# Kernel tuning notes

Measured on AMD Instinct MI355X. Metric: run time of the kernel, lower is better.

## Reference

```python
import jax, jax.numpy as jnp
import numpy as np

B, S, H = 2, 1024, 1024
NH, HD = 8, 128
E, TOPK, MI = 8, 2, 1024
SI = 2 * MI  # shared experts intermediate (n_shared_experts=2)
EPS = 1e-6
THETA = 10000.0


def setup_inputs() -> dict:
    key = jax.random.key(0)
    ks = jax.random.split(key, 16)
    w = lambda k, shp: (0.02 * jax.random.normal(k, shp, dtype=jnp.float32))
    # RoPE tables [S, HD]
    inv_freq = 1.0 / (THETA ** (np.arange(0, HD, 2, dtype=np.float32) / HD))
    t = np.arange(S, dtype=np.float32)
    freqs = np.outer(t, inv_freq)
    emb = np.concatenate([freqs, freqs], axis=-1)
    return {
        "hidden_states": jax.random.normal(ks[0], (B, S, H), dtype=jnp.float32),
        "ln1_w": jnp.ones((H,), jnp.float32),
        "ln2_w": jnp.ones((H,), jnp.float32),
        "q_w": w(ks[1], (H, H)),
        "k_w": w(ks[2], (H, H)),
        "v_w": w(ks[3], (H, H)),
        "o_w": w(ks[4], (H, H)),
        "cos": jnp.asarray(np.cos(emb), jnp.float32),
        "sin": jnp.asarray(np.sin(emb), jnp.float32),
        "gate_w": w(ks[5], (E, H)),
        "eg_w": w(ks[6], (E, MI, H)),
        "eu_w": w(ks[7], (E, MI, H)),
        "ed_w": w(ks[8], (E, H, MI)),
        "sg_w": w(ks[9], (SI, H)),
        "su_w": w(ks[10], (SI, H)),
        "sd_w": w(ks[11], (H, SI)),
    }


def _rmsnorm(x, w):
    return x * jax.lax.rsqrt(jnp.mean(x * x, axis=-1, keepdims=True) + EPS) * w


def _rotate_half(x):
    x1, x2 = jnp.split(x, 2, axis=-1)
    return jnp.concatenate([-x2, x1], axis=-1)


def _attention(x, q_w, k_w, v_w, o_w, cos, sin):
    b, s, h = x.shape
    q = (x @ q_w.T).reshape(b, s, NH, HD)
    k = (x @ k_w.T).reshape(b, s, NH, HD)
    v = (x @ v_w.T).reshape(b, s, NH, HD)
    c = cos[None, :s, None, :]
    sn = sin[None, :s, None, :]
    q = q * c + _rotate_half(q) * sn
    k = k * c + _rotate_half(k) * sn
    scores = jnp.einsum("bqhd,bkhd->bhqk", q, k) / jnp.sqrt(jnp.float32(HD))
    causal = jnp.tril(jnp.ones((s, s), dtype=bool))
    scores = jnp.where(causal[None, None], scores, -jnp.inf)
    p = jax.nn.softmax(scores, axis=-1)
    out = jnp.einsum("bhqk,bkhd->bqhd", p, v).reshape(b, s, h)
    return out @ o_w.T


def _mlp(x, gw, uw, dw):
    return (jax.nn.silu(x @ gw.T) * (x @ uw.T)) @ dw.T


def _moe(x, gate_w, eg_w, eu_w, ed_w, sg_w, su_w, sd_w):
    b, s, h = x.shape
    xt = x.reshape(-1, h)                              # [T, H]
    T = xt.shape[0]
    probs = jax.nn.softmax(xt @ gate_w.T, axis=-1)     # [T, E]
    rw, idx = jax.lax.top_k(probs, TOPK)               # [T, K]
    rw = rw / (jnp.sum(rw, axis=-1, keepdims=True) + 1e-20)  # norm_topk_prob
    # dense combine weights [T, E] (zero for unselected experts)
    w_full = jnp.zeros((T, E), xt.dtype).at[jnp.arange(T)[:, None], idx].add(rw)
    # dense all-expert compute, masked-combined (faithful to per-token loop math)
    g = jax.nn.silu(jnp.einsum("th,eih->tei", xt, eg_w))
    u = jnp.einsum("th,eih->tei", xt, eu_w)
    y = jnp.einsum("tei,ehi->teh", g * u, ed_w)        # [T, E, H]
    routed = jnp.einsum("teh,te->th", y, w_full)
    shared = _mlp(xt, sg_w, su_w, sd_w)
    return (routed + shared).reshape(b, s, h)


def reference(hidden_states, ln1_w, ln2_w, q_w, k_w, v_w, o_w, cos, sin,
              gate_w, eg_w, eu_w, ed_w, sg_w, su_w, sd_w):
    x = hidden_states
    x = x + _attention(_rmsnorm(x, ln1_w), q_w, k_w, v_w, o_w, cos, sin)
    x = x + _moe(_rmsnorm(x, ln2_w), gate_w, eg_w, eu_w, ed_w, sg_w, su_w, sd_w)
    return x
```

## Files before the change

### kernel.cpp

```cpp
#include <hip/hip_runtime.h>

#define B_   2
#define S_   1024
#define H_   1024
#define NH_  8
#define HD_  128
#define E_   8
#define MI_  1024
#define SI_  2048
#define T_   2048
#define CAP_ 2048

typedef unsigned short u16;
typedef __attribute__((ext_vector_type(4))) float f32x4;
typedef __attribute__((ext_vector_type(4))) unsigned short u16x4;
typedef __attribute__((ext_vector_type(8))) unsigned short u16x8;
typedef __attribute__((ext_vector_type(8))) __bf16 bf16x8;

__device__ __forceinline__ u16 f2bf(float f) {
  unsigned int u = __builtin_bit_cast(unsigned int, f);
  u = (u + 0x7fffu + ((u >> 16) & 1u)) >> 16;
  return (u16)u;
}
__device__ __forceinline__ float bf2f(u16 u) {
  return __builtin_bit_cast(float, (unsigned int)u << 16);
}
__device__ __forceinline__ float wave_sum(float v) {
#pragma unroll
  for (int o = 32; o; o >>= 1) v += __shfl_down(v, o, 64);
  return v;
}
__device__ __forceinline__ void gll16(const u16* g, u16* l) {
  __builtin_amdgcn_global_load_lds((const __attribute__((address_space(1))) void*)g,
                                   (__attribute__((address_space(3))) void*)l, 16, 0, 0);
}

__device__ __forceinline__ void cvt_moe_rows(
    int row0, int tid,
    const float* __restrict__ eg_w, const float* __restrict__ eu_w,
    const float* __restrict__ ed_w, const float* __restrict__ sg_w,
    const float* __restrict__ su_w, const float* __restrict__ sd_w,
    u16* __restrict__ egu, u16* __restrict__ edb,
    u16* __restrict__ sgu, u16* __restrict__ sdb) {
  const float* src[8];
  u16* dst[8];
#pragma unroll
  for (int g = 0; g < 8; g++) {
    int row = row0 + g;
    if (row < 20480) {
      int rel = row - 4096;
      int zu = rel >= 8192;
      int r = rel & 8191;
      int e = r >> 10, i = r & 1023;
      int orow = (i >> 4) * 32 + (i & 15) + (zu ? 16 : 0);
      src[g] = (zu ? eu_w : eg_w) + (long)r * 1024;
      dst[g] = egu + ((long)e * 2048 + orow) * 1024;
    } else if (row < 28672) {
      long f = (long)(row - 20480) * 1024;
      src[g] = ed_w + f;
      dst[g] = edb + f;
    } else if (row < 32768) {
      int rel = row - 28672;
      int zu = rel >= 2048;
      int i = rel & 2047;
      int orow = (i >> 4) * 32 + (i & 15) + (zu ? 16 : 0);
      src[g] = (zu ? su_w : sg_w) + (long)i * 1024;
      dst[g] = sgu + (long)orow * 1024;
    } else {
      long f = (long)(row - 32768) * 1024;
      src[g] = sd_w + f;
      dst[g] = sdb + f;
    }
  }
  f32x4 v[8];
#pragma unroll
  for (int g = 0; g < 8; g++)
    v[g] = __builtin_nontemporal_load((const f32x4*)src[g] + tid);
#pragma unroll
  for (int g = 0; g < 8; g++) {
    u16x4 o;
#pragma unroll
    for (int c = 0; c < 4; c++) o[c] = f2bf(v[g][c]);
    ((u16x4*)dst[g])[tid] = o;
  }
}

__global__ void cvt_all(const float* __restrict__ q_w, const float* __restrict__ k_w,
                        const float* __restrict__ v_w, const float* __restrict__ o_w,
                        u16* __restrict__ qwb,
                        const float* __restrict__ hidden, const float* __restrict__ ln1w,
                        u16* __restrict__ xn) {
  int bid = blockIdx.x, tid = threadIdx.x;
  if (bid >= 512) {
    int t = bid - 512;
    f32x4 v = ((const f32x4*)(hidden + (long)t * H_))[tid];
    float ss = v[0]*v[0] + v[1]*v[1] + v[2]*v[2] + v[3]*v[3];
    __shared__ float red[4];
    float s = wave_sum(ss);
    if ((tid & 63) == 0) red[tid >> 6] = s;
    __syncthreads();
    float r = rsqrtf((red[0] + red[1] + red[2] + red[3]) * (1.0f / H_) + 1e-6f);
    f32x4 wv = ((const f32x4*)ln1w)[tid];
    u16x4 o;
#pragma unroll
    for (int c = 0; c < 4; c++) o[c] = f2bf(v[c] * r * wv[c]);
    ((u16x4*)(xn + (long)t * H_))[tid] = o;
    return;
  }
  const float* src[8];
  u16* dst[8];
#pragma unroll
  for (int g = 0; g < 8; g++) {
    int row = bid * 8 + g;
    int seg = row >> 10;
    const float* in = (seg == 0) ? q_w : (seg == 1) ? k_w : (seg == 2) ? v_w : o_w;
    src[g] = in + (long)(row & 1023) * 1024;
    dst[g] = qwb + (long)row * 1024;
  }
  f32x4 v[8];
#pragma unroll
  for (int g = 0; g < 8; g++)
    v[g] = __builtin_nontemporal_load((const f32x4*)src[g] + tid);
#pragma unroll
  for (int g = 0; g < 8; g++) {
    u16x4 o;
#pragma unroll
    for (int c = 0; c < 4; c++) o[c] = f2bf(v[g][c]);
    ((u16x4*)dst[g])[tid] = o;
  }
}

__global__ void rmsnorm2_gate(const float* __restrict__ x1, const float* __restrict__ ln2w,
                              const float* __restrict__ gw, u16* __restrict__ xn,
                              int* __restrict__ eidx, float* __restrict__ aw) {
  int t = blockIdx.x, tid = threadIdx.x;
  int lane = tid & 63, wave = tid >> 6;
  f32x4 v = ((const f32x4*)(x1 + (long)t * H_))[tid];
  float ss = v[0]*v[0] + v[1]*v[1] + v[2]*v[2] + v[3]*v[3];
  __shared__ float redS[4];
  __shared__ float redE[4][E_];
  float s = wave_sum(ss);
  if (lane == 0) redS[wave] = s;
  __syncthreads();
  float r = rsqrtf((redS[0] + redS[1] + redS[2] + redS[3]) * (1.0f / H_) + 1e-6f);
  f32x4 wv = ((const f32x4*)ln2w)[tid];
  float xv[4];
  u16x4 o;
#pragma unroll
  for (int c = 0; c < 4; c++) { xv[c] = v[c] * r * wv[c]; o[c] = f2bf(xv[c]); }
  ((u16x4*)(xn + (long)t * H_))[tid] = o;
  float acc[E_];
#pragma unroll
  for (int e = 0; e < E_; e++) {
    f32x4 g = ((const f32x4*)(gw + (long)e * H_))[tid];
    acc[e] = xv[0]*g[0] + xv[1]*g[1] + xv[2]*g[2] + xv[3]*g[3];
  }
#pragma unroll
  for (int e = 0; e < E_; e++) acc[e] = wave_sum(acc[e]);
  if (lane == 0)
#pragma unroll
    for (int e = 0; e < E_; e++) redE[wave][e] = acc[e];
  __syncthreads();
  if (tid == 0) {
    float l[E_];
#pragma unroll
    for (int e = 0; e < E_; e++) l[e] = redE[0][e] + redE[1][e] + redE[2][e] + redE[3][e];
    float mx = l[0];
#pragma unroll
    for (int e = 1; e < E_; e++) mx = fmaxf(mx, l[e]);
    float p[E_], z = 0.f;
#pragma unroll
    for (int e = 0; e < E_; e++) { p[e] = __expf(l[e] - mx); z += p[e]; }
    int e0 = 0;
#pragma unroll
    for (int e = 1; e < E_; e++) if (p[e] > p[e0]) e0 = e;
    int e1 = (e0 == 0) ? 1 : 0;
#pragma unroll
    for (int e = 0; e < E_; e++) if (e != e0 && p[e] > p[e1]) e1 = e;
    float q0 = p[e0] / z, q1 = p[e1] / z;
    float invs = 1.0f / (q0 + q1 + 1e-20f);
    eidx[t * 2] = e0;
    eidx[t * 2 + 1] = e1;
    aw[t * 2] = q0 * invs;
    aw[t * 2 + 1] = q1 * invs;
  }
}

__global__ __launch_bounds__(256) void route_scan(const int* __restrict__ eidx,
                                                  int* __restrict__ arow,
                                                  int* __restrict__ cursor,
                                                  int* __restrict__ itok,
                                                  int* __restrict__ wgu,
                                                  int* __restrict__ wdn) {
  __shared__ int sc[E_][256];
  int tid = threadIdx.x;
  for (int i = tid; i < E_ * CAP_; i += 256) itok[i] = 0;
  unsigned c0 = 0, c1 = 0;
  int ebuf[16];
#pragma unroll
  for (int i = 0; i < 16; i++) {
    int e = eidx[tid * 16 + i];
    ebuf[i] = e;
    if (e < 4) c0 += 1u << (8 * e); else c1 += 1u << (8 * (e - 4));
  }
#pragma unroll
  for (int e = 0; e < E_; e++)
    sc[e][tid] = (e < 4) ? (int)((c0 >> (8 * e)) & 0xff) : (int)((c1 >> (8 * (e - 4))) & 0xff);
  __syncthreads();
  for (int st = 1; st < 256; st <<= 1) {
    int v[E_];
#pragma unroll
    for (int e = 0; e < E_; e++) v[e] = (tid >= st) ? sc[e][tid - st] : 0;
    __syncthreads();
#pragma unroll
    for (int e = 0; e < E_; e++) sc[e][tid] += v[e];
    __syncthreads();
  }
  for (int i = tid; i < 640; i += 256) wgu[i] = -1;
  for (int i = tid; i < 1152; i += 256) wdn[i] = -1;
  __syncthreads();
  if (tid < 8) cursor[tid] = sc[tid][255];
  for (int i = tid; i < 512; i += 256) {
    int e = i >> 6, item = i & 63;
    int mt = item >> 3, nx = item & 7;
    int nmt = (min(sc[e][255], CAP_) + 255) >> 8;
    if (mt < nmt) wgu[e + 8 * (mt * 8 + nx)] = (0 << 12) | (e << 8) | (mt << 4) | nx;
  }
  if (tid < 128) {
    int k = tid >> 4, idx = tid & 15;
    int mi = idx >> 2, ni = idx & 3;
    int nmt = (min(sc[k][255], CAP_) + 255) >> 8;
    wgu[k + 8 * (8 * nmt + idx)] = (1 << 12) | ((4 * (k >> 2) + mi) << 4) | (4 * (k & 3) + ni);
  }
  for (int i = tid; i < 1024; i += 256) {
    int e = i >> 7, item = i & 127;
    int mt = item >> 3, nx = item & 7;
    int nmt = (min(sc[e][255], CAP_) + 127) >> 7;
    if (mt < nmt) wdn[e + 8 * (mt * 8 + nx)] = (0 << 16) | (e << 12) | (mt << 5) | nx;
  }
  if (tid < 128) {
    int k = tid >> 4, idx = tid & 15;
    int mi = idx >> 2, ni = idx & 3;
    int nmt = (min(sc[k][255], CAP_) + 127) >> 7;
    wdn[k + 8 * (8 * nmt + idx)] = (1 << 16) | ((4 * (k >> 1) + mi) << 5) | (4 * (k & 1) + ni);
  }
  int base[E_];
#pragma unroll
  for (int e = 0; e < E_; e++) {
    int own = (e < 4) ? (int)((c0 >> (8 * e)) & 0xff) : (int)((c1 >> (8 * (e - 4))) & 0xff);
    base[e] = sc[e][tid] - own;
  }
  __syncthreads();
#pragma unroll
  for (int e = 0; e < E_; e++) sc[e][tid] = base[e];
  __syncthreads();
  unsigned r0 = 0, r1 = 0;
#pragma unroll
  for (int i = 0; i < 16; i++) {
    int e = ebuf[i];
    int run = (e < 4) ? (int)((r0 >> (8 * e)) & 0xff) : (int)((r1 >> (8 * (e - 4))) & 0xff);
    int row = e * CAP_ + sc[e][tid] + run;
    arow[tid * 16 + i] = row;
    itok[row] = (tid * 16 + i) >> 1;
    if (e < 4) r0 += 1u << (8 * e); else r1 += 1u << (8 * (e - 4));
  }
}

__global__ void rope_vtrans(const u16* __restrict__ qkvb, const float* __restrict__ cs,
                            const float* __restrict__ sn, u16* __restrict__ qb,
                            u16* __restrict__ kb, u16* __restrict__ vt) {
  int bid = blockIdx.x, tid = threadIdx.x;
  if (bid < 1024) {
    int z = bid >> 9;
    const u16* src = qkvb + (long)z * 2097152;
    u16* dstb = z ? kb : qb;
    int rb = (bid & 511) * 32 + (tid >> 3);
    int u = tid & 7;
    int h = rb & 7, bs = rb >> 3, s = bs & 1023, b = bs >> 10;
    const u16* row = src + (long)rb * 128;
    int d0 = u * 8;
    u16x8 v1 = *(const u16x8*)(row + d0);
    u16x8 v2 = *(const u16x8*)(row + d0 + 64);
    const float* c1 = cs + s * 128 + d0;
    const float* s1 = sn + s * 128 + d0;
    u16x8 o1, o2;
#pragma unroll
    for (int c = 0; c < 8; c++) {
      float a = bf2f(v1[c]), q2 = bf2f(v2[c]);
      o1[c] = f2bf(a * c1[c] - q2 * s1[c]);
      o2[c] = f2bf(q2 * c1[c + 64] + a * s1[c + 64]);
    }
    u16* orow = dstb + ((long)((b * NH_ + h) * S_ + s)) * HD_;
    *(u16x8*)(orow + d0) = o1;
    *(u16x8*)(orow + d0 + 64) = o2;
  } else {
    int vb = bid - 1024;
    int bh = vb >> 5;
    int rem = vb & 31;
    int s0 = (rem >> 1) * 64, d0 = (rem & 1) * 64;
    int b = bh >> 3, h = bh & 7;
    __shared__ u16 tile[64][68];
    const u16* vsrc = qkvb + 2 * 2097152;
#pragma unroll
    for (int it = 0; it < 4; it++) {
      int idx = it * 256 + tid;
      int r = idx >> 4, c = (idx & 15) * 4;
      u16x4 vv = *(const u16x4*)(vsrc + (((long)(b * S_ + s0 + r)) * NH_ + h) * HD_ + d0 + c);
      *(u16x4*)&tile[r][c] = vv;
    }
    __syncthreads();
#pragma unroll
    for (int it = 0; it < 4; it++) {
      int idx = it * 256 + tid;
      int dr = idx >> 4, sc = (idx & 15) * 4;
      u16x4 ov;
#pragma unroll
      for (int k = 0; k < 4; k++) ov[k] = tile[sc + k][dr];
      *(u16x4*)(vt + ((long)bh * HD_ + d0 + dr) * S_ + s0 + sc) = ov;
    }
  }
}

__global__ __launch_bounds__(256) void flash_cvt(
    const u16* __restrict__ qb, const u16* __restrict__ kb,
    const u16* __restrict__ vt, u16* __restrict__ Po,
    float* __restrict__ Pm, float* __restrict__ Pl,
    const float* __restrict__ eg_w, const float* __restrict__ eu_w,
    const float* __restrict__ ed_w, const float* __restrict__ sg_w,
    const float* __restrict__ su_w, const float* __restrict__ sd_w,
    u16* __restrict__ egu, u16* __restrict__ edb,
    u16* __restrict__ sgu, u16* __restrict__ sdb) {
  int bid = blockIdx.x;
  int tid = threadIdx.x;
  if (bid >= 640) {
    int row0 = 4096 + (bid - 640) * 8;
    cvt_moe_rows(row0, tid, eg_w, eu_w, ed_w, sg_w, su_w, sd_w, egu, edb, sgu, sdb);
    return;
  }
  int item = bid % 40;
  int bh = bid / 40;
  int qt, ch;
  if (item < 4)       { qt = item;                    ch = 0; }
  else if (item < 12) { qt = 4 + ((item - 4) >> 1);   ch = (item - 4) & 1; }
  else if (item < 24) { qt = 8 + (item - 12) / 3;     ch = (item - 12) % 3; }
  else                { qt = 12 + ((item - 24) >> 2); ch = (item - 24) & 3; }
  int j0 = ch * 4, j1 = min(j0 + 4, qt + 1);

  int wavei = tid >> 6, lane = tid & 63;
  int la = lane & 15, qd = lane >> 4;

  __shared__ __align__(16) u16 Ks[64 * 128];
  __shared__ __align__(16) u16 Vs[128 * 64];
  __shared__ __align__(16) u16 Ps[4][16 * 64];

  bf16x8 qf[4];
  const u16* qrow = qb + ((long)bh * S_ + qt * 64 + wavei * 16 + la) * HD_;
#pragma unroll
  for (int ks = 0; ks < 4; ks++)
    qf[ks] = *(const bf16x8*)(qrow + ks * 32 + qd * 8);

  f32x4 oacc[8];
#pragma unroll
  for (int nf = 0; nf < 8; nf++) oacc[nf] = (f32x4){0.f, 0.f, 0.f, 0.f};
  float m_i[4], l_i[4];
#pragma unroll
  for (int r = 0; r < 4; r++) { m_i[r] = -1e30f; l_i[r] = 0.f; }

  const u16* Kbase = kb + (long)bh * S_ * HD_;
  const u16* Vbase = vt + (long)bh * HD_ * S_;
  const float scale = 0.08838834764831845f;
  u16* pw = (u16*)Ps[wavei];
  int swz = la & 7;

  for (int j = j0; j < j1; j++) {
    __syncthreads();
#pragma unroll
    for (int t = 0; t < 4; t++) {
      int blk = t * 4 + wavei;
      int kr = blk * 4 + (lane >> 4);
      int kc = (lane & 15) ^ (kr & 7);
      gll16(Kbase + ((long)j * 64 + kr) * 128 + kc * 8, Ks + blk * 512);
      int vr = blk * 8 + (lane >> 3);
      int vc = (lane & 7) ^ (vr & 7);
      gll16(Vbase + (long)vr * 1024 + j * 64 + vc * 8, Vs + blk * 512);
    }
    __syncthreads();

    f32x4 sacc[4];
#pragma unroll
    for (int jf = 0; jf < 4; jf++) sacc[jf] = (f32x4){0.f, 0.f, 0.f, 0.f};
#pragma unroll
    for (int ks = 0; ks < 4; ks++)
#pragma unroll
      for (int jf = 0; jf < 4; jf++) {
        bf16x8 kfrag = *(const bf16x8*)(Ks + (jf * 16 + la) * 128 + ((ks * 4 + qd) ^ swz) * 8);
        sacc[jf] = __builtin_amdgcn_mfma_f32_16x16x32_bf16(qf[ks], kfrag, sacc[jf], 0, 0, 0);
      }

    float sv[4][4];
    int qglob = qt * 64 + wavei * 16 + qd * 4;
#pragma unroll
    for (int jf = 0; jf < 4; jf++) {
      int kglob = j * 64 + jf * 16 + la;
#pragma unroll
      for (int r = 0; r < 4; r++)
        sv[jf][r] = (kglob <= qglob + r) ? sacc[jf][r] * scale : -1e30f;
    }
    float mnew[4], alpha[4];
#pragma unroll
    for (int r = 0; r < 4; r++) {
      float mx = fmaxf(fmaxf(sv[0][r], sv[1][r]), fmaxf(sv[2][r], sv[3][r]));
#pragma unroll
      for (int o = 1; o < 16; o <<= 1) mx = fmaxf(mx, __shfl_xor(mx, o, 64));
      mnew[r] = fmaxf(m_i[r], mx);
      alpha[r] = __expf(m_i[r] - mnew[r]);
      m_i[r] = mnew[r];
    }
#pragma unroll
    for (int r = 0; r < 4; r++) {
      float sum = 0.f;
#pragma unroll
      for (int jf = 0; jf < 4; jf++) {
        float p = __expf(sv[jf][r] - mnew[r]);
        sv[jf][r] = p;
        sum += p;
      }
#pragma unroll
      for (int o = 1; o < 16; o <<= 1) sum += __shfl_xor(sum, o, 64);
      l_i[r] = l_i[r] * alpha[r] + sum;
    }
#pragma unroll
    for (int jf = 0; jf < 4; jf++)
#pragma unroll
      for (int r = 0; r < 4; r++) {
        int rp = qd * 4 + r;
        int e = jf * 16 + la;
        pw[rp * 64 + (((e >> 3) ^ (rp & 7)) << 3) + (e & 7)] = f2bf(sv[jf][r]);
      }
#pragma unroll
    for (int nf = 0; nf < 8; nf++)
#pragma unroll
      for (int r = 0; r < 4; r++) oacc[nf][r] *= alpha[r];
#pragma unroll
    for (int ks = 0; ks < 2; ks++) {
      bf16x8 pfrag = *(const bf16x8*)(pw + la * 64 + ((ks * 4 + qd) ^ swz) * 8);
#pragma unroll
      for (int nf = 0; nf < 8; nf++) {
        bf16x8 vfrag = *(const bf16x8*)(Vs + (nf * 16 + la) * 64 + (((ks * 4 + qd) & 7) ^ swz) * 8);
        oacc[nf] = __builtin_amdgcn_mfma_f32_16x16x32_bf16(pfrag, vfrag, oacc[nf], 0, 0, 0);
      }
    }
  }

  int pidx = (bh * 16 + qt) * 4 + ch;
  int rowb = wavei * 16 + qd * 4;
  u16* pob = Po + ((long)pidx * 64 + rowb) * 128;
#pragma unroll
  for (int r = 0; r < 4; r++)
#pragma unroll
    for (int nf = 0; nf < 8; nf++)
      pob[(long)r * 128 + nf * 16 + la] = f2bf(oacc[nf][r]);
  if (la == 0)
#pragma unroll
    for (int r = 0; r < 4; r++) {
      Pm[pidx * 64 + rowb + r] = m_i[r];
      Pl[pidx * 64 + rowb + r] = l_i[r];
    }
}

__global__ __launch_bounds__(256) void attn_merge(
    const u16* __restrict__ Po, const float* __restrict__ Pm,
    const float* __restrict__ Pl, u16* __restrict__ attn) {
  int qt = blockIdx.x, bh = blockIdx.y;
  int b = bh >> 3, h = bh & 7;
  int nch = (qt >> 2) + 1;
  int t = threadIdx.x;
  int row = t >> 2, cg = (t & 3) * 32;
  long base = (long)(bh * 16 + qt) * 4;
  float mv[4], wv[4];
  float M = -1e30f;
  for (int c = 0; c < nch; c++) { mv[c] = Pm[(base + c) * 64 + row]; M = fmaxf(M, mv[c]); }
  float L = 0.f;
  for (int c = 0; c < nch; c++) { wv[c] = __expf(mv[c] - M); L += wv[c] * Pl[(base + c) * 64 + row]; }
  float inv = 1.0f / L;
  f32x4 o[8];
#pragma unroll
  for (int k = 0; k < 8; k++) o[k] = (f32x4){0.f, 0.f, 0.f, 0.f};
  for (int c = 0; c < nch; c++) {
    const u16x4* src = (const u16x4*)(Po + ((base + c) * 64 + row) * 128 + cg);
#pragma unroll
    for (int k = 0; k < 8; k++) {
      u16x4 sv = src[k];
#pragma unroll
      for (int e = 0; e < 4; e++) o[k][e] += bf2f(sv[e]) * wv[c];
    }
  }
  u16* dst = attn + ((long)b * S_ + qt * 64 + row) * H_ + h * HD_ + cg;
#pragma unroll
  for (int k = 0; k < 8; k++) {
    u16x4 ov;
#pragma unroll
    for (int c = 0; c < 4; c++) ov[c] = f2bf(o[k][c] * inv);
    ((u16x4*)dst)[k] = ov;
  }
}

__global__ void final_combine(const float* __restrict__ x1, const float* __restrict__ ys,
                              const u16* __restrict__ y, const int* __restrict__ arow,
                              const float* __restrict__ aw, float* __restrict__ out) {
  int t = blockIdx.x;
  int i = threadIdx.x * 4;
  int r0 = arow[t * 2], r1 = arow[t * 2 + 1];
  float w0 = aw[t * 2], w1 = aw[t * 2 + 1];
  f32x4 a = *(const f32x4*)(x1 + (long)t * H_ + i);
  f32x4 b = *(const f32x4*)(ys + (long)t * H_ + i);
  u16x4 y0 = *(const u16x4*)(y + (long)r0 * H_ + i);
  u16x4 y1 = *(const u16x4*)(y + (long)r1 * H_ + i);
  f32x4 o;
#pragma unroll
  for (int c = 0; c < 4; c++)
    o[c] = a[c] + b[c] + w0 * bf2f(y0[c]) + w1 * bf2f(y1[c]);
  *(f32x4*)(out + (long)t * H_ + i) = o;
}

__global__ __launch_bounds__(512) void gemm256(
    const u16* __restrict__ Ag, const u16* __restrict__ Bg, u16* __restrict__ Cg,
    int K, int lda, int ldb, int ldc, long sBz, long sCz,
    const int* __restrict__ itok, const int* __restrict__ wgu,
    const u16* __restrict__ Bg2, u16* __restrict__ Cg2,
    int ldb2, int ldc2) {
  int s = wgu[blockIdx.x];
  if (s < 0) return;
  int kind = s >> 12;
  int z = (s >> 8) & 7;
  int m0 = ((s >> 4) & 15) << 8;
  int n0 = (s & 15) << 8;
  const u16* A = Ag;
  const u16* B;
  u16* C;
  long cbase;
  bool ind;
  if (kind) { B = Bg2; C = Cg2; ldb = ldb2; ldc = ldc2; cbase = 0; ind = false; }
  else      { B = Bg + (long)z * sBz; C = Cg; cbase = (long)z * sCz; ind = true; }

  __shared__ __align__(16) u16 As[2][256 * 64];
  __shared__ __align__(16) u16 Bs[2][256 * 64];
  int tid = threadIdx.x;
  int lane = tid & 63, wave = tid >> 6;
  int wr = wave >> 2, wc = wave & 3;
  int wm = wr * 128, wn = wc * 64;
  int la = lane & 15, qd = lane >> 4;
  int sr = lane >> 3;
  int scs = (lane & 7) ^ (sr & 7);

  const u16* ap[4];
  const u16* bp[4];
#pragma unroll
  for (int r = 0; r < 4; r++) {
    int rloc = m0 + r * 64 + wave * 8 + sr;
    long arow_g = ind ? (long)itok[(long)z * CAP_ + rloc] : (long)rloc;
    ap[r] = A + arow_g * lda + scs * 8;
    bp[r] = B + (long)(n0 + r * 64 + wave * 8 + sr) * ldb + scs * 8;
  }

  f32x4 acc[8][4];
#pragma unroll
  for (int i = 0; i < 8; i++)
#pragma unroll
    for (int j = 0; j < 4; j++) acc[i][j] = (f32x4){0.f, 0.f, 0.f, 0.f};

  auto stage = [&](int buf, int k0) {
#pragma unroll
    for (int r = 0; r < 4; r++)
      gll16(ap[r] + k0, &As[buf][(r * 64 + wave * 8) * 64]);
#pragma unroll
    for (int r = 0; r < 4; r++)
      gll16(bp[r] + k0, &Bs[buf][(r * 64 + wave * 8) * 64]);
  };

  int sw = la & 7;
  int nt = K >> 6;
  int cur = 0;
  stage(0, 0);
  for (int t = 0; t < nt; ++t) {
    if (t + 1 < nt) {
      stage(cur ^ 1, (t + 1) * 64);
      asm volatile("s_waitcnt vmcnt(8)" ::: "memory");
    } else {
      asm volatile("s_waitcnt vmcnt(0)" ::: "memory");
    }
    __builtin_amdgcn_s_barrier();
#pragma unroll
    for (int kk = 0; kk < 2; kk++) {
      bf16x8 af[8], bfv[4];
#pragma unroll
      for (int i = 0; i < 8; i++)
        af[i] = *(const bf16x8*)(&As[cur][0] + (wm + i * 16 + la) * 64 + (((kk * 4 + qd) ^ sw) << 3));
#pragma unroll
      for (int j = 0; j < 4; j++)
        bfv[j] = *(const bf16x8*)(&Bs[cur][0] + (wn + j * 16 + la) * 64 + (((kk * 4 + qd) ^ sw) << 3));
#pragma unroll
      for (int i = 0; i < 8; i++)
#pragma unroll
        for (int j = 0; j < 4; j++)
          acc[i][j] = __builtin_amdgcn_mfma_f32_16x16x32_bf16(af[i], bfv[j], acc[i][j], 0, 0, 0);
    }
    __builtin_amdgcn_s_barrier();
    cur ^= 1;
  }

#pragma unroll
  for (int i = 0; i < 8; i++) {
#pragma unroll
    for (int jp = 0; jp < 2; jp++) {
      int hcol = ((n0 + wn) >> 1) + (jp << 4) + la;
#pragma unroll
      for (int r = 0; r < 4; r++) {
        int row = m0 + wm + i * 16 + qd * 4 + r;
        float g = acc[i][jp * 2][r], u = acc[i][jp * 2 + 1][r];
        float sg = g / (1.f + __expf(-g));
        C[cbase + (long)row * ldc + hcol] = f2bf(sg * u);
      }
    }
  }
}

template <int MT, int STORE_BF16, int ADD_RES, int FUSE_SILU, int IND, int WL>
__global__ __launch_bounds__(256) void gemm_bt(
    const u16* __restrict__ Ag, const u16* __restrict__ Bg, void* __restrict__ Cg,
    const float* __restrict__ Res, int K, int lda, int ldb, int ldc,
    long sAz, long sBz, long sCz, const int* __restrict__ mlimit,
    const int* __restrict__ itok, const int* __restrict__ wlist,
    const u16* __restrict__ Ag2, const u16* __restrict__ Bg2, void* __restrict__ Cg2,
    int lda2, int ldb2, int ldc2, int K2) {
  constexpr int MR = MT / 32;
  int z = 0, m0, n0, kind = 0;
  const u16 *A, *B;
  void* C;
  long cbase;
  bool ind = (IND != 0);
  if constexpr (WL == 3) {
    int s = wlist[blockIdx.x];
    if (s < 0) return;
    kind = s >> 16;
    m0 = ((s >> 5) & 127) * MT;
    n0 = (s & 31) * 128;
    if (kind) {
      A = Ag2; B = Bg2; C = Cg2;
      lda = lda2; ldb = ldb2; ldc = ldc2; K = K2;
      ind = false;
      cbase = 0;
    } else {
      z = (s >> 12) & 7;
      A = Ag + (IND ? 0 : z * sAz);
      B = Bg + z * sBz;
      C = Cg;
      cbase = (long)z * sCz;
    }
  } else {
    z = blockIdx.z;
    m0 = blockIdx.y * MT;
    n0 = blockIdx.x * 128;
    if (mlimit && m0 >= mlimit[z]) return;
    A = Ag + (IND ? 0 : z * sAz);
    B = Bg + z * sBz;
    C = Cg;
    cbase = (long)z * sCz;
  }

  __shared__ __align__(16) u16 As[2][MT * 64];
  __shared__ __align__(16) u16 Bs[2][128 * 64];
  int tid = threadIdx.x;
  int lane = tid & 63, wave = tid >> 6;
  int wm = (wave & 1) * (MT / 2), wn = (wave >> 1) * 64;
  int la = lane & 15, qd = lane >> 4;
  int sr = lane >> 3;
  int scs = (lane & 7) ^ (sr & 7);

  const u16* ap[MT / 32];
  const u16* bp[4];
#pragma unroll
  for (int t = 0; t < MT / 32; t++) {
    int rloc = m0 + t * 32 + wave * 8 + sr;
    long arow_g = (IND && ind) ? (long)itok[(long)z * CAP_ + rloc] : (long)rloc;
    ap[t] = A + arow_g * lda + scs * 8;
  }
#pragma unroll
  for (int t = 0; t < 4; t++)
    bp[t] = B + (long)(n0 + t * 32 + wave * 8 + sr) * ldb + scs * 8;

  f32x4 acc[MR][4];
#pragma unroll
  for (int i = 0; i < MR; i++)
#pragma unroll
    for (int j = 0; j < 4; j++) acc[i][j] = (f32x4){0.f, 0.f, 0.f, 0.f};

  auto stage = [&](int buf, int k0) {
#pragma unroll
    for (int t = 0; t < MT / 32; t++)
      gll16(ap[t] + k0, &As[buf][(t * 32 + wave * 8) * 64]);
#pragma unroll
    for (int t = 0; t < 4; t++)
      gll16(bp[t] + k0, &Bs[buf][(t * 32 + wave * 8) * 64]);
  };

  int sw = la & 7;
  int nt = K >> 6;
  int cur = 0;
  stage(0, 0);
  for (int t = 0; t < nt; ++t) {
    if (t + 1 < nt) {
      stage(cur ^ 1, (t + 1) * 64);
      if constexpr (MT == 128)
        asm volatile("s_waitcnt vmcnt(8)" ::: "memory");
      else
        asm volatile("s_waitcnt vmcnt(6)" ::: "memory");
    } else {
      asm volatile("s_waitcnt vmcnt(0)" ::: "memory");
    }
    __builtin_amdgcn_s_barrier();
#pragma unroll
    for (int kk = 0; kk < 2; kk++) {
      bf16x8 af[MR], bfv[4];
#pragma unroll
      for (int i = 0; i < MR; i++)
        af[i] = *(const bf16x8*)(&As[cur][0] + (wm + i * 16 + la) * 64 + (((kk * 4 + qd) ^ sw) << 3));
#pragma unroll
      for (int j = 0; j < 4; j++)
        bfv[j] = *(const bf16x8*)(&Bs[cur][0] + (wn + j * 16 + la) * 64 + (((kk * 4 + qd) ^ sw) << 3));
#pragma unroll
      for (int i = 0; i < MR; i++)
#pragma unroll
        for (int j = 0; j < 4; j++)
          acc[i][j] = __builtin_amdgcn_mfma_f32_16x16x32_bf16(af[i], bfv[j], acc[i][j], 0, 0, 0);
    }
    __builtin_amdgcn_s_barrier();
    cur ^= 1;
  }

  if (FUSE_SILU) {
#pragma unroll
    for (int i = 0; i < MR; i++) {
#pragma unroll
      for (int jp = 0; jp < 2; jp++) {
        int hcol = ((n0 + wn) >> 1) + (jp << 4) + la;
#pragma unroll
        for (int r = 0; r < 4; r++) {
          int row = m0 + wm + i * 16 + qd * 4 + r;
          float g = acc[i][jp * 2][r], u = acc[i][jp * 2 + 1][r];
          float sg = g / (1.f + __expf(-g));
          ((u16*)C)[cbase + (long)row * ldc + hcol] = f2bf(sg * u);
        }
      }
    }
  } else {
    bool sbf = (WL >= 2) ? (kind == 0) : (STORE_BF16 != 0);
#pragma unroll
    for (int i = 0; i < MR; i++) {
#pragma unroll
      for (int j = 0; j < 4; j++) {
        int col = n0 + wn + j * 16 + la;
#pragma unroll
        for (int r = 0; r < 4; r++) {
          int row = m0 + wm + i * 16 + qd * 4 + r;
          float v = acc[i][j][r];
          long ci = cbase + (long)row * ldc + col;
          if (ADD_RES) v += Res[(long)row * ldc + col];
          if (sbf) ((u16*)C)[ci] = f2bf(v);
          else ((float*)C)[ci] = v;
        }
      }
    }
  }
}

extern "C" void kernel_launch(void* const* d_in, const int* in_sizes, int n_in,
                              void* d_out, int out_size, void* d_ws, size_t ws_size,
                              hipStream_t stream) {
  const float* hidden = (const float*)d_in[0];
  const float* ln1w = (const float*)d_in[1];
  const float* ln2w = (const float*)d_in[2];
  const float* q_w = (const float*)d_in[3];
  const float* k_w = (const float*)d_in[4];
  const float* v_w = (const float*)d_in[5];
  const float* o_w = (const float*)d_in[6];
  const float* cosp = (const float*)d_in[7];
  const float* sinp = (const float*)d_in[8];
  const float* gate_w = (const float*)d_in[9];
  const float* eg_w = (const float*)d_in[10];
  const float* eu_w = (const float*)d_in[11];
  const float* ed_w = (const float*)d_in[12];
  const float* sg_w = (const float*)d_in[13];
  const float* su_w = (const float*)d_in[14];
  const float* sd_w = (const float*)d_in[15];
  float* out = (float*)d_out;

  char* w = (char*)d_ws;
  const size_t MB = 1u << 20;
  u16* qwb = (u16*)(w + 0 * MB);
  u16* egu = (u16*)(w + 8 * MB);
  u16* edb = (u16*)(w + 40 * MB);
  u16* sgu = (u16*)(w + 56 * MB);
  u16* sdb = (u16*)(w + 64 * MB);
  float* x1 = (float*)(w + 68 * MB);
  u16* xn = (u16*)(w + 76 * MB);
  u16* attn = (u16*)(w + 80 * MB);
  int* cursor = (int*)(w + 84 * MB);
  int* arow = (int*)(w + 84 * MB + 1024);
  float* aw = (float*)(w + 84 * MB + 20 * 1024);
  int* eidx = (int*)(w + 84 * MB + 40 * 1024);
  int* itok = (int*)(w + 84 * MB + 60 * 1024);
  int* wgu = (int*)(w + 84 * MB + 132 * 1024);
  int* wdn = (int*)(w + 84 * MB + 136 * 1024);
  u16* qkvb = (u16*)(w + 85 * MB);
  u16* qb = (u16*)(w + 109 * MB);
  u16* kb = (u16*)(w + 113 * MB);
  u16* vt = (u16*)(w + 117 * MB);
  u16* Po = (u16*)(w + 121 * MB);
  float* Pm = (float*)(w + 155 * MB);
  float* Pl = (float*)(w + 156 * MB);
  u16* hbuf = (u16*)(w + 121 * MB);
  u16* y = (u16*)(w + 157 * MB);
  u16* hs = (u16*)(w + 189 * MB);
  float* ys = (float*)(w + 197 * MB);

  const long M1 = 1048576, M2 = 2097152;

  cvt_all<<<2560, 256, 0, stream>>>(q_w, k_w, v_w, o_w, qwb, hidden, ln1w, xn);

  gemm_bt<128, 1, 0, 0, 0, 0><<<dim3(8, 16, 3), 256, 0, stream>>>(
      xn, qwb, qkvb, nullptr, 1024, 1024, 1024, 1024, 0, M1, M2, nullptr, nullptr,
      nullptr, nullptr, nullptr, nullptr, 0, 0, 0, 0);
  rope_vtrans<<<1536, 256, 0, stream>>>(qkvb, cosp, sinp, qb, kb, vt);
  flash_cvt<<<640 + 3840, 256, 0, stream>>>(qb, kb, vt, Po, Pm, Pl,
                                            eg_w, eu_w, ed_w, sg_w, su_w, sd_w,
                                            egu, edb, sgu, sdb);
  attn_merge<<<dim3(16, 16), 256, 0, stream>>>(Po, Pm, Pl, attn);
  gemm_bt<64, 0, 1, 0, 0, 0><<<dim3(8, 32, 1), 256, 0, stream>>>(
      attn, qwb + 3 * M1, x1, hidden, 1024, 1024, 1024, 1024, 0, 0, 0, nullptr, nullptr,
      nullptr, nullptr, nullptr, nullptr, 0, 0, 0, 0);

  rmsnorm2_gate<<<T_, 256, 0, stream>>>(x1, ln2w, gate_w, xn, eidx, aw);
  route_scan<<<1, 256, 0, stream>>>(eidx, arow, cursor, itok, wgu, wdn);
  gemm256<<<640, 512, 0, stream>>>(
      xn, egu, hbuf, 1024, 1024, 1024, MI_,
      (long)2 * MI_ * H_, (long)CAP_ * MI_, itok, wgu,
      sgu, hs, 1024, SI_);
  gemm_bt<128, 1, 0, 0, 0, 3><<<1152, 256, 0, stream>>>(
      hbuf, edb, y, nullptr, 1024, 1024, 1024, 1024,
      (long)CAP_ * MI_, (long)H_ * MI_, (long)CAP_ * H_, nullptr, nullptr, wdn,
      hs, sdb, ys, 2048, 2048, 1024, 2048);

  final_combine<<<T_, 256, 0, stream>>>(x1, ys, y, arow, aw, out);
}
```

Measured before the change: 375.8 us.

## Move down-proj weight conversion into gate/up GEMM launch and fuse residual into shared-expert output

The fp32-to-bf16 conversion of the expert and shared down-projection weights moves out of the flash-attention launch and into extra blocks appended to the gate/up GEMM launch. This shortens the attention-phase kernel and lets the conversion overlap the grouped GEMM. The down GEMM now adds the x1 residual directly into the shared-expert output written to `out`, so final_combine no longer reads the separate fp32 ys buffer. The risk is that the conversion blocks compete with the gate/up GEMM for bandwidth and compute slots. Correctness also depends on the conversion blocks finishing before the next kernel reads edb and sdb, which stream ordering gives.

```diff
diff --git a/kernel.cpp b/kernel.cpp
--- a/kernel.cpp
+++ b/kernel.cpp
@@ -35,41 +35,30 @@
                                    (__attribute__((address_space(3))) void*)l, 16, 0, 0);
 }
 
-__device__ __forceinline__ void cvt_moe_rows(
-    int row0, int tid,
+__device__ __forceinline__ void cvt_gu_rows(
+    int cvtid, int tid,
     const float* __restrict__ eg_w, const float* __restrict__ eu_w,
-    const float* __restrict__ ed_w, const float* __restrict__ sg_w,
-    const float* __restrict__ su_w, const float* __restrict__ sd_w,
-    u16* __restrict__ egu, u16* __restrict__ edb,
-    u16* __restrict__ sgu, u16* __restrict__ sdb) {
+    const float* __restrict__ sg_w, const float* __restrict__ su_w,
+    u16* __restrict__ egu, u16* __restrict__ sgu) {
   const float* src[8];
   u16* dst[8];
 #pragma unroll
   for (int g = 0; g < 8; g++) {
-    int row = row0 + g;
-    if (row < 20480) {
-      int rel = row - 4096;
+    if (cvtid < 2048) {
+      int rel = cvtid * 8 + g;
       int zu = rel >= 8192;
       int r = rel & 8191;
       int e = r >> 10, i = r & 1023;
       int orow = (i >> 4) * 32 + (i & 15) + (zu ? 16 : 0);
       src[g] = (zu ? eu_w : eg_w) + (long)r * 1024;
       dst[g] = egu + ((long)e * 2048 + orow) * 1024;
-    } else if (row < 28672) {
-      long f = (long)(row - 20480) * 1024;
-      src[g] = ed_w + f;
-      dst[g] = edb + f;
-    } else if (row < 32768) {
-      int rel = row - 28672;
+    } else {
+      int rel = (cvtid - 2048) * 8 + g;
       int zu = rel >= 2048;
       int i = rel & 2047;
       int orow = (i >> 4) * 32 + (i & 15) + (zu ? 16 : 0);
       src[g] = (zu ? su_w : sg_w) + (long)i * 1024;
       dst[g] = sgu + (long)orow * 1024;
-    } else {
-      long f = (long)(row - 32768) * 1024;
-      src[g] = sd_w + f;
-      dst[g] = sdb + f;
     }
   }
   f32x4 v[8];
@@ -82,6 +71,27 @@
 #pragma unroll
     for (int c = 0; c < 4; c++) o[c] = f2bf(v[g][c]);
     ((u16x4*)dst[g])[tid] = o;
+  }
+}
+
+__device__ __forceinline__ void cvt_d_rows(
+    int grp, int tid,
+    const float* __restrict__ ed_w, const float* __restrict__ sd_w,
+    u16* __restrict__ edb, u16* __restrict__ sdb) {
+  const float* src;
+  u16* dst;
+  if (grp < 1024) { long f = (long)grp * 8192; src = ed_w + f; dst = edb + f; }
+  else            { long f = (long)(grp - 1024) * 8192; src = sd_w + f; dst = sdb + f; }
+  f32x4 v[8];
+#pragma unroll
+  for (int g = 0; g < 8; g++)
+    v[g] = __builtin_nontemporal_load((const f32x4*)(src + g * 1024) + tid);
+#pragma unroll
+  for (int g = 0; g < 8; g++) {
+    u16x4 o;
+#pragma unroll
+    for (int c = 0; c < 4; c++) o[c] = f2bf(v[g][c]);
+    ((u16x4*)(dst + g * 1024))[tid] = o;
   }
 }
 
@@ -326,15 +336,12 @@
     const u16* __restrict__ vt, u16* __restrict__ Po,
     float* __restrict__ Pm, float* __restrict__ Pl,
     const float* __restrict__ eg_w, const float* __restrict__ eu_w,
-    const float* __restrict__ ed_w, const float* __restrict__ sg_w,
-    const float* __restrict__ su_w, const float* __restrict__ sd_w,
-    u16* __restrict__ egu, u16* __restrict__ edb,
-    u16* __restrict__ sgu, u16* __restrict__ sdb) {
+    const float* __restrict__ sg_w, const float* __restrict__ su_w,
+    u16* __restrict__ egu, u16* __restrict__ sgu) {
   int bid = blockIdx.x;
   int tid = threadIdx.x;
   if (bid >= 640) {
-    int row0 = 4096 + (bid - 640) * 8;
-    cvt_moe_rows(row0, tid, eg_w, eu_w, ed_w, sg_w, su_w, sd_w, egu, edb, sgu, sdb);
+    cvt_gu_rows(bid - 640, tid, eg_w, eu_w, sg_w, su_w, egu, sgu);
     return;
   }
   int item = bid % 40;
@@ -505,21 +512,19 @@
   }
 }
 
-__global__ void final_combine(const float* __restrict__ x1, const float* __restrict__ ys,
-                              const u16* __restrict__ y, const int* __restrict__ arow,
+__global__ void final_combine(const u16* __restrict__ y, const int* __restrict__ arow,
                               const float* __restrict__ aw, float* __restrict__ out) {
   int t = blockIdx.x;
   int i = threadIdx.x * 4;
   int r0 = arow[t * 2], r1 = arow[t * 2 + 1];
   float w0 = aw[t * 2], w1 = aw[t * 2 + 1];
-  f32x4 a = *(const f32x4*)(x1 + (long)t * H_ + i);
-  f32x4 b = *(const f32x4*)(ys + (long)t * H_ + i);
+  f32x4 a = *(const f32x4*)(out + (long)t * H_ + i);
   u16x4 y0 = *(const u16x4*)(y + (long)r0 * H_ + i);
   u16x4 y1 = *(const u16x4*)(y + (long)r1 * H_ + i);
   f32x4 o;
 #pragma unroll
   for (int c = 0; c < 4; c++)
-    o[c] = a[c] + b[c] + w0 * bf2f(y0[c]) + w1 * bf2f(y1[c]);
+    o[c] = a[c] + w0 * bf2f(y0[c]) + w1 * bf2f(y1[c]);
   *(f32x4*)(out + (long)t * H_ + i) = o;
 }
 
@@ -528,8 +533,17 @@
     int K, int lda, int ldb, int ldc, long sBz, long sCz,
     const int* __restrict__ itok, const int* __restrict__ wgu,
     const u16* __restrict__ Bg2, u16* __restrict__ Cg2,
-    int ldb2, int ldc2) {
-  int s = wgu[blockIdx.x];
+    int ldb2, int ldc2,
+    const float* __restrict__ ed_w, const float* __restrict__ sd_w,
+    u16* __restrict__ edb, u16* __restrict__ sdb) {
+  int bid = blockIdx.x;
+  int tid = threadIdx.x;
+  if (bid >= 640) {
+    int grp = (bid - 640) * 2 + (tid >= 256 ? 1 : 0);
+    cvt_d_rows(grp, tid & 255, ed_w, sd_w, edb, sdb);
+    return;
+  }
+  int s = wgu[bid];
   if (s < 0) return;
   int kind = s >> 12;
   int z = (s >> 8) & 7;
@@ -545,7 +559,6 @@
 
   __shared__ __align__(16) u16 As[2][256 * 64];
   __shared__ __align__(16) u16 Bs[2][256 * 64];
-  int tid = threadIdx.x;
   int lane = tid & 63, wave = tid >> 6;
   int wr = wave >> 2, wc = wave & 3;
   int wm = wr * 128, wn = wc * 64;
@@ -755,6 +768,7 @@
     }
   } else {
     bool sbf = (WL >= 2) ? (kind == 0) : (STORE_BF16 != 0);
+    bool addres = ADD_RES && (WL != 3 || kind == 1);
 #pragma unroll
     for (int i = 0; i < MR; i++) {
 #pragma unroll
@@ -765,7 +779,7 @@
           int row = m0 + wm + i * 16 + qd * 4 + r;
           float v = acc[i][j][r];
           long ci = cbase + (long)row * ldc + col;
-          if (ADD_RES) v += Res[(long)row * ldc + col];
+          if (addres) v += Res[(long)row * ldc + col];
           if (sbf) ((u16*)C)[ci] = f2bf(v);
           else ((float*)C)[ci] = v;
         }
@@ -822,7 +836,6 @@
   u16* hbuf = (u16*)(w + 121 * MB);
   u16* y = (u16*)(w + 157 * MB);
   u16* hs = (u16*)(w + 189 * MB);
-  float* ys = (float*)(w + 197 * MB);
 
   const long M1 = 1048576, M2 = 2097152;
 
@@ -832,9 +845,8 @@
       xn, qwb, qkvb, nullptr, 1024, 1024, 1024, 1024, 0, M1, M2, nullptr, nullptr,
       nullptr, nullptr, nullptr, nullptr, 0, 0, 0, 0);
   rope_vtrans<<<1536, 256, 0, stream>>>(qkvb, cosp, sinp, qb, kb, vt);
-  flash_cvt<<<640 + 3840, 256, 0, stream>>>(qb, kb, vt, Po, Pm, Pl,
-                                            eg_w, eu_w, ed_w, sg_w, su_w, sd_w,
-                                            egu, edb, sgu, sdb);
+  flash_cvt<<<640 + 2560, 256, 0, stream>>>(qb, kb, vt, Po, Pm, Pl,
+                                            eg_w, eu_w, sg_w, su_w, egu, sgu);
   attn_merge<<<dim3(16, 16), 256, 0, stream>>>(Po, Pm, Pl, attn);
   gemm_bt<64, 0, 1, 0, 0, 0><<<dim3(8, 32, 1), 256, 0, stream>>>(
       attn, qwb + 3 * M1, x1, hidden, 1024, 1024, 1024, 1024, 0, 0, 0, nullptr, nullptr,
@@ -842,14 +854,14 @@
 
   rmsnorm2_gate<<<T_, 256, 0, stream>>>(x1, ln2w, gate_w, xn, eidx, aw);
   route_scan<<<1, 256, 0, stream>>>(eidx, arow, cursor, itok, wgu, wdn);
-  gemm256<<<640, 512, 0, stream>>>(
+  gemm256<<<640 + 640, 512, 0, stream>>>(
       xn, egu, hbuf, 1024, 1024, 1024, MI_,
       (long)2 * MI_ * H_, (long)CAP_ * MI_, itok, wgu,
-      sgu, hs, 1024, SI_);
-  gemm_bt<128, 1, 0, 0, 0, 3><<<1152, 256, 0, stream>>>(
-      hbuf, edb, y, nullptr, 1024, 1024, 1024, 1024,
+      sgu, hs, 1024, SI_, ed_w, sd_w, edb, sdb);
+  gemm_bt<128, 1, 1, 0, 0, 3><<<1152, 256, 0, stream>>>(
+      hbuf, edb, y, x1, 1024, 1024, 1024, 1024,
       (long)CAP_ * MI_, (long)H_ * MI_, (long)CAP_ * H_, nullptr, nullptr, wdn,
-      hs, sdb, ys, 2048, 2048, 1024, 2048);
-
-  final_combine<<<T_, 256, 0, stream>>>(x1, ys, y, arow, aw, out);
-}
+      hs, sdb, out, 2048, 2048, 1024, 2048);
+
+  final_combine<<<T_, 256, 0, stream>>>(y, arow, aw, out);
+}
```

Measured after the change: 382.4 us. About the same (+1.8%).
